# Performance work log

Measured on AMD Instinct MI355X. Metric: run time of the kernel, lower is better.

The kernel has to match this reference:

```python
import jax, jax.numpy as jnp
import numpy as np

B, R, C, E, H = 2, 16, 512, 1024, 16
D = E // H  # head_dim = 64


def setup_inputs() -> dict:
    key = jax.random.key(0)
    ks = jax.random.split(key, 9)
    s = 1.0 / np.sqrt(E)
    return {
        "x": jax.random.normal(ks[0], (B, R, C, E), dtype=jnp.float32),
        "wq": jax.random.uniform(ks[1], (E, E), jnp.float32, -s, s),
        "bq": jax.random.uniform(ks[2], (E,), jnp.float32, -s, s),
        "wk": jax.random.uniform(ks[3], (E, E), jnp.float32, -s, s),
        "bk": jax.random.uniform(ks[4], (E,), jnp.float32, -s, s),
        "wv": jax.random.uniform(ks[5], (E, E), jnp.float32, -s, s),
        "bv": jax.random.uniform(ks[6], (E,), jnp.float32, -s, s),
        "wo": jax.random.uniform(ks[7], (E, E), jnp.float32, -s, s),
        "bo": jax.random.uniform(ks[8], (E,), jnp.float32, -s, s),
    }


def reference(x, wq, bq, wk, bk, wv, bv, wo, bo):
    b, r, c, e = x.shape
    # projections: [b,r,c,e] -> [b,r,h,c,d]
    def split_heads(t):
        return t.reshape(b, r, c, H, D).transpose(0, 1, 3, 2, 4)
    q = split_heads(x @ wq + bq)
    k = split_heads(x @ wk + bk)
    v = split_heads(x @ wv + bv)
    scale = 1.0 / jnp.sqrt(jnp.asarray(D, x.dtype))
    logits = jnp.einsum('brhqd,brhkd->brhqk', q, k) * scale
    probs = jax.nn.softmax(logits, axis=-1)
    ctx = jnp.einsum('brhqk,brhkd->brhqd', probs, v)
    ctx = ctx.transpose(0, 1, 3, 2, 4).reshape(b, r, c, e)
    return ctx @ wo + bo
```

## Files before the change

kernel.cpp:

```cpp
#include <hip/hip_runtime.h>
#include <hip/hip_bf16.h>
#include <hip/hip_fp16.h>
#include <math.h>

typedef _Float16 half8 __attribute__((ext_vector_type(8)));
typedef __attribute__((ext_vector_type(4))) float floatx4;

constexpr int Bc = 2, Rc = 16, Cc = 512, Ec = 1024, Hc = 16, Dc = 64;
#define QSCALE 0.180336880111120425f

__device__ inline void gl_lds16(const void* g, void* l) {
  __builtin_amdgcn_global_load_lds(
      (const __attribute__((address_space(1))) void*)g,
      (__attribute__((address_space(3))) void*)l, 16, 0, 0);
}
__device__ inline unsigned short f2h(float f) {
  __half h = __float2half_rn(f);
  return *(unsigned short*)&h;
}
__device__ inline unsigned int pack_h2(float lo, float hi) {
  __half2 p = __float22half2_rn(make_float2(lo, hi));
  return *(unsigned int*)&p;
}

__global__ __launch_bounds__(256) void cvt_x(const float* __restrict__ x,
                                             unsigned short* __restrict__ xh) {
  const size_t base = ((size_t)blockIdx.x * 256 + threadIdx.x) * 8;
  float4 a = *(const float4*)(x + base);
  float4 b = *(const float4*)(x + base + 4);
  uint4 o;
  o.x = pack_h2(a.x, a.y);
  o.y = pack_h2(a.z, a.w);
  o.z = pack_h2(b.x, b.y);
  o.w = pack_h2(b.z, b.w);
  *(uint4*)(xh + base) = o;
}

__global__ __launch_bounds__(256) void wprep(
    const float* __restrict__ w0, const float* __restrict__ w1,
    const float* __restrict__ w2, const float* __restrict__ w3,
    unsigned short* __restrict__ t0, unsigned short* __restrict__ t1,
    unsigned short* __restrict__ t2, unsigned short* __restrict__ t3) {
  __shared__ float tile[64][65];
  const int z = blockIdx.z;
  const float* W = (z == 0) ? w0 : (z == 1) ? w1 : (z == 2) ? w2 : w3;
  unsigned short* T = (z == 0) ? t0 : (z == 1) ? t1 : (z == 2) ? t2 : t3;
  const int tid = threadIdx.x;
  const int bk = blockIdx.x * 64, bn = blockIdx.y * 64;
#pragma unroll
  for (int p = 0; p < 16; ++p) {
    int idx = p * 256 + tid;
    int lk = idx >> 6, lnn = idx & 63;
    tile[lnn][lk] = W[(size_t)(bk + lk) * 1024 + bn + lnn];
  }
  __syncthreads();
  const int lane = tid & 63, sub = tid >> 6;
  const int lr = lane & 15, quad = lane >> 4;
#pragma unroll
  for (int tl = 0; tl < 2; ++tl) {
    float v[8];
#pragma unroll
    for (int jj = 0; jj < 8; ++jj)
      v[jj] = tile[sub * 16 + lr][tl * 32 + quad * 8 + jj];
    uint4 o;
    o.x = pack_h2(v[0], v[1]);
    o.y = pack_h2(v[2], v[3]);
    o.z = pack_h2(v[4], v[5]);
    o.w = pack_h2(v[6], v[7]);
    const size_t n16 = (size_t)(bn >> 4) + sub;
    const size_t tt = (size_t)(bk >> 5) + tl;
    *(uint4*)(T + ((n16 * 32 + tt) * 64 + lane) * 8) = o;
  }
}

#define WAIT_VM(N)                                                            \
  {                                                                           \
    __builtin_amdgcn_sched_barrier(0);                                        \
    asm volatile("s_waitcnt vmcnt(" #N ")" ::: "memory");                     \
    __builtin_amdgcn_sched_barrier(0);                                        \
  }

#define STG_A(SBUF, KT)                                                       \
  {                                                                           \
    _Pragma("unroll") for (int l_ = 0; l_ < 2; ++l_) {                        \
      const int r0_ = l_ * 128 + w * 16;                                      \
      gl_lds16(Ab + (size_t)r0_ * 1024 + glan + (size_t)(KT) * 32,            \
               As + (SBUF) * 8192 + r0_ * 32);                                \
    }                                                                         \
  }

#define BLOAD(FB, KT)                                                         \
  _Pragma("unroll") for (int j_ = 0; j_ < 4; ++j_) FB[j_] =                   \
      *(const half8*)(Bf + bqoff + (size_t)j_ * 16384 + (size_t)(KT) * 512);

#define DSRA(NBUF, FA)                                                        \
  _Pragma("unroll") for (int i_ = 0; i_ < 8; ++i_) FA[i_] =                   \
      *(const half8*)&As[(NBUF) * 8192 + (wm + i_ * 16 + lr) * 32 + swq];

#define MFMA32(FA, FB)                                                        \
  _Pragma("unroll") for (int i_ = 0; i_ < 8; ++i_)                            \
      _Pragma("unroll") for (int j_ = 0; j_ < 4; ++j_) acc[i_][j_] =          \
          __builtin_amdgcn_mfma_f32_16x16x32_f16(FA[i_], FB[j_],              \
                                                 acc[i_][j_], 0, 0, 0);

#define TSTEP(NBUF, SBUF, KSTG, KBLD, FA, FB, NFA, NFB, STGE, BLDE, DSRE,     \
              VMN, BARE)                                                      \
  {                                                                           \
    if (STGE) STG_A(SBUF, KSTG);                                              \
    if (BLDE) BLOAD(NFB, KBLD);                                               \
    if (DSRE) DSRA(NBUF, NFA);                                                \
    WAIT_VM(VMN);                                                             \
    __builtin_amdgcn_s_setprio(1);                                            \
    MFMA32(FA, FB);                                                           \
    __builtin_amdgcn_s_setprio(0);                                            \
    if (BARE) {                                                               \
      __builtin_amdgcn_s_barrier();                                           \
      __builtin_amdgcn_sched_barrier(0);                                      \
    }                                                                         \
  }

template <int MODE>
__global__ __launch_bounds__(512, 2) void gemm256(
    const unsigned short* __restrict__ gA, const unsigned short* __restrict__ gB,
    const float* __restrict__ bq, const float* __restrict__ bk,
    const float* __restrict__ bv, unsigned short* __restrict__ qout,
    unsigned short* __restrict__ kout, unsigned short* __restrict__ vout,
    float* __restrict__ fout, const float* __restrict__ bo) {
  __shared__ unsigned short As[4 * 8192];
  const int tid = threadIdx.x;
  const int w = tid >> 6, ln = tid & 63;
  const int lr = ln & 15, quad = ln >> 4;
  const int wm = (w >> 2) * 128, wn = (w & 3) * 64;
  int bm, bn;
  if (MODE == 0) {
    const int swz = (blockIdx.x & 7) * 96 + (blockIdx.x >> 3);
    bm = (swz / 12) * 256;
    bn = (swz % 12) * 256;
  } else {
    const int swz = (blockIdx.x & 7) * 32 + (blockIdx.x >> 3);
    bm = (swz >> 2) * 256;
    bn = (swz & 3) * 256;
  }
  const unsigned short* Ab = gA + (size_t)bm * 1024;
  const unsigned short* Bf = gB;
  const size_t bqoff =
      (size_t)((bn >> 4) + (w & 3) * 4) * 16384 + (size_t)ln * 8;
  const int glan = (ln >> 2) * 1024 + (((ln & 3) ^ ((ln >> 3) & 3)) << 3);
  const int swq = ((quad ^ ((lr >> 1) & 3)) << 3);

  floatx4 acc[8][4];
#pragma unroll
  for (int i = 0; i < 8; ++i)
#pragma unroll
    for (int j = 0; j < 4; ++j) acc[i][j] = (floatx4)(0.f);
  half8 fa0[8], fa1[8], fb0[4], fb1[4];

  STG_A(0, 0);
  STG_A(1, 1);
  STG_A(2, 2);
  BLOAD(fb0, 0);
  WAIT_VM(6);
  __builtin_amdgcn_s_barrier();
  __builtin_amdgcn_sched_barrier(0);
  DSRA(0, fa0);

  for (int tt = 0; tt < 7; ++tt) {
    const int k4 = tt * 4;
    TSTEP(1, 3, k4 + 3, k4 + 1, fa0, fb0, fa1, fb1, 1, 1, 1, 6, 1);
    TSTEP(2, 0, k4 + 4, k4 + 2, fa1, fb1, fa0, fb0, 1, 1, 1, 6, 1);
    TSTEP(3, 1, k4 + 5, k4 + 3, fa0, fb0, fa1, fb1, 1, 1, 1, 6, 1);
    TSTEP(0, 2, k4 + 6, k4 + 4, fa1, fb1, fa0, fb0, 1, 1, 1, 6, 1);
  }
  TSTEP(1, 3, 31, 29, fa0, fb0, fa1, fb1, 1, 1, 1, 6, 1);
  TSTEP(2, 0, 0, 30, fa1, fb1, fa0, fb0, 0, 1, 1, 4, 1);
  TSTEP(3, 0, 0, 31, fa0, fb0, fa1, fb1, 0, 1, 1, 4, 1);
  TSTEP(0, 0, 0, 0, fa1, fb1, fa0, fb0, 0, 0, 0, 0, 0);

  const int q4 = quad * 4;
  const bool odd = ln & 1;
  if constexpr (MODE == 0) {
    const int z = bn >> 10;
    const float* bias = (z == 0) ? bq : (z == 1) ? bk : bv;
    const int czb = (bn & 1023) + wn;
#pragma unroll
    for (int i = 0; i < 8; ++i) {
#pragma unroll
      for (int j = 0; j < 4; ++j) {
        const int colz = czb + j * 16 + lr;
        float v[4];
#pragma unroll
        for (int r = 0; r < 4; ++r) v[r] = acc[i][j][r] + bias[colz];
        const int m0 = bm + wm + i * 16 + q4;
        const int h = colz >> 6, d = colz & 63;
        const int brr = m0 >> 9, c0 = m0 & 511;
        const size_t hb = ((size_t)brr * 16 + h) * 32768;
        if (z == 2) {
          uint2 o;
          o.x = pack_h2(v[0], v[1]);
          o.y = pack_h2(v[2], v[3]);
          *(uint2*)(vout + hb + (size_t)d * 512 + c0) = o;
        } else {
          unsigned short* outp = (z == 0) ? qout : kout;
          if (z == 0) {
#pragma unroll
            for (int r = 0; r < 4; ++r) v[r] *= QSCALE;
          }
#pragma unroll
          for (int rp = 0; rp < 2; ++rp) {
            float a = v[2 * rp], b = v[2 * rp + 1];
            float ax = __shfl_xor(a, 1), bx = __shfl_xor(b, 1);
            unsigned int u = odd ? pack_h2(bx, b) : pack_h2(a, ax);
            const int c = c0 + 2 * rp + (odd ? 1 : 0);
            const int dd = d & ~1;
            *(unsigned int*)(outp + hb + (size_t)c * 64 + dd) = u;
          }
        }
      }
    }
  } else {
#pragma unroll
    for (int i = 0; i < 8; ++i)
#pragma unroll
      for (int j = 0; j < 4; ++j) {
        const int col = bn + wn + j * 16 + lr;
#pragma unroll
        for (int r = 0; r < 4; ++r) {
          const int m = bm + wm + i * 16 + q4 + r;
          fout[(size_t)m * 1024 + col] = acc[i][j][r] + bo[col];
        }
      }
  }
}

__global__ __launch_bounds__(256, 2) void attn_mfma(
    const unsigned short* __restrict__ Qh, const unsigned short* __restrict__ Kb,
    const unsigned short* __restrict__ Vt, unsigned short* __restrict__ Ctx) {
  __shared__ unsigned short Ks[128 * 64];
  __shared__ unsigned short Vs[64 * 128];
  __shared__ unsigned short Ps[128][136];

  const int t = threadIdx.x;
  const int w = t >> 6, ln = t & 63;
  const int lane15 = ln & 15, quad = ln >> 4;
  const bool odd = ln & 1;
  const int bh = blockIdx.x >> 2;
  const int qb = (blockIdx.x & 3) * 128;

  half8 qf[2][2];
  {
    const size_t qbase =
        ((size_t)bh * 512 + qb + w * 32 + lane15) * 64 + quad * 8;
#pragma unroll
    for (int i = 0; i < 2; ++i)
#pragma unroll
      for (int c = 0; c < 2; ++c)
        qf[i][c] = *(const half8*)(Qh + qbase + (size_t)i * 16 * 64 + c * 32);
  }

  floatx4 oacc[2][4];
#pragma unroll
  for (int i = 0; i < 2; ++i)
#pragma unroll
    for (int dj = 0; dj < 4; ++dj) oacc[i][dj] = (floatx4)(0.f);
  float lsum[2][4];
#pragma unroll
  for (int i = 0; i < 2; ++i)
#pragma unroll
    for (int r = 0; r < 4; ++r) lsum[i][r] = 0.f;

  const unsigned short* kgb = Kb + (size_t)bh * 32768;
  const unsigned short* vgb = Vt + (size_t)bh * 32768;

  for (int kt = 0; kt < 512; kt += 128) {
    __syncthreads();
    {
      const unsigned short* kq = kgb + (size_t)kt * 64;
#pragma unroll
      for (int p = 0; p < 4; ++p) {
        const int s = p * 256 + t;
        const int kr = s >> 3, kc16 = s & 7;
        gl_lds16(kq + kr * 64 + ((kc16 ^ (kr & 7)) << 3), (char*)Ks + s * 16);
        const int vr = s >> 4, vc16 = s & 15;
        gl_lds16(vgb + vr * 512 + kt + ((vc16 ^ (vr & 15)) << 3),
                 (char*)Vs + s * 16);
      }
    }
    __syncthreads();

    floatx4 sacc[2][8];
#pragma unroll
    for (int i = 0; i < 2; ++i)
#pragma unroll
      for (int j = 0; j < 8; ++j) sacc[i][j] = (floatx4)(0.f);
#pragma unroll
    for (int j = 0; j < 8; ++j) {
      const int krow = j * 16 + lane15;
      const unsigned short* kr = Ks + krow * 64;
      half8 kf0 = *(const half8*)(kr + ((quad ^ (krow & 7)) << 3));
      half8 kf1 = *(const half8*)(kr + (((4 + quad) ^ (krow & 7)) << 3));
#pragma unroll
      for (int i = 0; i < 2; ++i) {
        sacc[i][j] = __builtin_amdgcn_mfma_f32_16x16x32_f16(qf[i][0], kf0,
                                                            sacc[i][j], 0, 0, 0);
        sacc[i][j] = __builtin_amdgcn_mfma_f32_16x16x32_f16(qf[i][1], kf1,
                                                            sacc[i][j], 0, 0, 0);
      }
    }

#pragma unroll
    for (int i = 0; i < 2; ++i) {
#pragma unroll
      for (int rp = 0; rp < 2; ++rp) {
        const int rA = rp * 2, rB = rA + 1;
        const int row = w * 32 + i * 16 + quad * 4 + rA + (odd ? 1 : 0);
        unsigned short* prow = &Ps[row][lane15 & ~1];
#pragma unroll
        for (int j = 0; j < 8; ++j) {
          const float pA = exp2f(sacc[i][j][rA]);
          const float pB = exp2f(sacc[i][j][rB]);
          lsum[i][rA] += pA;
          lsum[i][rB] += pB;
          const float an = __shfl_xor(pA, 1);
          const float bn = __shfl_xor(pB, 1);
          const float lo = odd ? bn : pA;
          const float hi = odd ? pB : an;
          *(unsigned int*)(prow + j * 16) = pack_h2(lo, hi);
        }
      }
    }

#pragma unroll
    for (int kc = 0; kc < 4; ++kc) {
      half8 pa0 = *(const half8*)&Ps[w * 32 + lane15][kc * 32 + quad * 8];
      half8 pa1 = *(const half8*)&Ps[w * 32 + 16 + lane15][kc * 32 + quad * 8];
#pragma unroll
      for (int dj = 0; dj < 4; ++dj) {
        const int drow = dj * 16 + lane15;
        half8 vf = *(const half8*)(
            Vs + drow * 128 + (((kc * 4 + quad) ^ (drow & 15)) << 3));
        oacc[0][dj] = __builtin_amdgcn_mfma_f32_16x16x32_f16(pa0, vf,
                                                             oacc[0][dj], 0, 0, 0);
        oacc[1][dj] = __builtin_amdgcn_mfma_f32_16x16x32_f16(pa1, vf,
                                                             oacc[1][dj], 0, 0, 0);
      }
    }
  }

  float invl[2][4];
#pragma unroll
  for (int i = 0; i < 2; ++i)
#pragma unroll
    for (int r = 0; r < 4; ++r) {
      float ls = lsum[i][r];
#pragma unroll
      for (int off = 1; off < 16; off <<= 1) ls += __shfl_xor(ls, off);
      invl[i][r] = 1.f / ls;
    }
  const int br = bh >> 4, h = bh & 15;
  const size_t mbase = (size_t)br * 512 + qb + w * 32;
#pragma unroll
  for (int i = 0; i < 2; ++i)
#pragma unroll
    for (int dj = 0; dj < 4; ++dj) {
      const int e = h * 64 + dj * 16 + lane15;
      const int ee = e & ~1;
#pragma unroll
      for (int rp = 0; rp < 2; ++rp) {
        const int rA = 2 * rp, rB = rA + 1;
        float a = oacc[i][dj][rA] * invl[i][rA];
        float b = oacc[i][dj][rB] * invl[i][rB];
        float ax = __shfl_xor(a, 1), bx = __shfl_xor(b, 1);
        unsigned int u = odd ? pack_h2(bx, b) : pack_h2(a, ax);
        const size_t m = mbase + i * 16 + quad * 4 + rA + (odd ? 1 : 0);
        *(unsigned int*)(Ctx + m * 1024 + ee) = u;
      }
    }
}

extern "C" void kernel_launch(void* const* d_in, const int* in_sizes, int n_in,
                              void* d_out, int out_size, void* d_ws,
                              size_t ws_size, hipStream_t stream) {
  const float* x = (const float*)d_in[0];
  const float* wq = (const float*)d_in[1];
  const float* bq = (const float*)d_in[2];
  const float* wk = (const float*)d_in[3];
  const float* bk = (const float*)d_in[4];
  const float* wv = (const float*)d_in[5];
  const float* bv = (const float*)d_in[6];
  const float* wo = (const float*)d_in[7];
  const float* bo = (const float*)d_in[8];
  float* out = (float*)d_out;

  char* w = (char*)d_ws;
  const size_t MiB = 1ull << 20;
  unsigned short* qbuf = (unsigned short*)(w + 0 * MiB);
  unsigned short* kbuf = (unsigned short*)(w + 32 * MiB);
  unsigned short* vtb = (unsigned short*)(w + 64 * MiB);
  unsigned short* xh = (unsigned short*)(w + 96 * MiB);
  unsigned short* ctx = (unsigned short*)(w + 128 * MiB);
  unsigned short* wqh = (unsigned short*)(w + 160 * MiB);
  unsigned short* wkh = (unsigned short*)(w + 162 * MiB);
  unsigned short* wvh = (unsigned short*)(w + 164 * MiB);
  unsigned short* woh = (unsigned short*)(w + 166 * MiB);

  cvt_x<<<8192, 256, 0, stream>>>(x, xh);
  wprep<<<dim3(16, 16, 4), 256, 0, stream>>>(wq, wk, wv, wo, wqh, wkh, wvh,
                                             woh);

  gemm256<0><<<768, 512, 0, stream>>>(xh, wqh, bq, bk, bv, qbuf, kbuf, vtb,
                                      nullptr, nullptr);

  attn_mfma<<<2048, 256, 0, stream>>>(qbuf, kbuf, vtb, ctx);

  gemm256<1><<<256, 512, 0, stream>>>(ctx, woh, nullptr, nullptr, nullptr,
                                      nullptr, nullptr, nullptr, out, bo);
}
```

Baseline: 371.8 us.

## Stage B operand through LDS with async loads and regroup block swizzle

Loads the B (weight) fragments into a new LDS ring buffer with global_load_lds instead of direct global-to-register loads, so both operands share one 4-slot async pipeline with a deeper prefetch distance. Waits on lgkmcnt are added before barriers, and the prologue stages four slots. The block-to-tile mapping is also changed so each XCD handles a contiguous group of M rows across a small set of N tiles, aiming for better L2 reuse. LDS use doubles, which may reduce occupancy, and the extra LDS round-trip for B adds ds_read traffic.

Result: slower. 431.5 us (+16.1%).

```diff
diff --git a/kernel.cpp b/kernel.cpp
--- a/kernel.cpp
+++ b/kernel.cpp
@@ -79,23 +79,34 @@
     asm volatile("s_waitcnt vmcnt(" #N ")" ::: "memory");                     \
     __builtin_amdgcn_sched_barrier(0);                                        \
   }
-
-#define STG_A(SBUF, KT)                                                       \
+#define WAIT_LGKM0                                                            \
+  {                                                                           \
+    asm volatile("s_waitcnt lgkmcnt(0)" ::: "memory");                        \
+    __builtin_amdgcn_sched_barrier(0);                                        \
+  }
+
+#define STG_AB(SLOT, KT)                                                      \
   {                                                                           \
     _Pragma("unroll") for (int l_ = 0; l_ < 2; ++l_) {                        \
       const int r0_ = l_ * 128 + w * 16;                                      \
       gl_lds16(Ab + (size_t)r0_ * 1024 + glan + (size_t)(KT) * 32,            \
-               As + (SBUF) * 8192 + r0_ * 32);                                \
+               As + (SLOT) * 8192 + r0_ * 32);                                \
     }                                                                         \
-  }
-
-#define BLOAD(FB, KT)                                                         \
-  _Pragma("unroll") for (int j_ = 0; j_ < 4; ++j_) FB[j_] =                   \
-      *(const half8*)(Bf + bqoff + (size_t)j_ * 16384 + (size_t)(KT) * 512);
-
-#define DSRA(NBUF, FA)                                                        \
-  _Pragma("unroll") for (int i_ = 0; i_ < 8; ++i_) FA[i_] =                   \
-      *(const half8*)&As[(NBUF) * 8192 + (wm + i_ * 16 + lr) * 32 + swq];
+    _Pragma("unroll") for (int l_ = 0; l_ < 2; ++l_) {                        \
+      const int fr_ = 2 * w + l_;                                             \
+      gl_lds16(Bf + (size_t)((n16b + fr_) * 32 + (KT)) * 512 + ln * 8,        \
+               Bs + (SLOT) * 8192 + fr_ * 512);                               \
+    }                                                                         \
+  }
+
+#define DSR(SLOT, FA, FB)                                                     \
+  {                                                                           \
+    _Pragma("unroll") for (int i_ = 0; i_ < 8; ++i_) FA[i_] =                 \
+        *(const half8*)&As[(SLOT) * 8192 + (wm + i_ * 16 + lr) * 32 + swq];   \
+    _Pragma("unroll") for (int j_ = 0; j_ < 4; ++j_) FB[j_] =                 \
+        *(const half8*)&Bs[(SLOT) * 8192 + ((w & 3) * 4 + j_) * 512 +         \
+                           ln * 8];                                           \
+  }
 
 #define MFMA32(FA, FB)                                                        \
   _Pragma("unroll") for (int i_ = 0; i_ < 8; ++i_)                            \
@@ -103,17 +114,18 @@
           __builtin_amdgcn_mfma_f32_16x16x32_f16(FA[i_], FB[j_],              \
                                                  acc[i_][j_], 0, 0, 0);
 
-#define TSTEP(NBUF, SBUF, KSTG, KBLD, FA, FB, NFA, NFB, STGE, BLDE, DSRE,     \
-              VMN, BARE)                                                      \
+#define TSTEP(DSLOT, SSLOT, KSTG, FA, FB, NFA, NFB, STGE, DSRE, VMW, BARE)    \
   {                                                                           \
-    if (STGE) STG_A(SBUF, KSTG);                                              \
-    if (BLDE) BLOAD(NFB, KBLD);                                               \
-    if (DSRE) DSRA(NBUF, NFA);                                                \
-    WAIT_VM(VMN);                                                             \
+    if (STGE) { STG_AB(SSLOT, KSTG); }                                        \
+    if (DSRE) { DSR(DSLOT, NFA, NFB); }                                       \
+    if ((VMW) == 0) { WAIT_VM(8); }                                           \
+    else if ((VMW) == 1) { WAIT_VM(4); }                                      \
+    else if ((VMW) == 2) { WAIT_VM(0); }                                      \
     __builtin_amdgcn_s_setprio(1);                                            \
     MFMA32(FA, FB);                                                           \
     __builtin_amdgcn_s_setprio(0);                                            \
     if (BARE) {                                                               \
+      WAIT_LGKM0;                                                             \
       __builtin_amdgcn_s_barrier();                                           \
       __builtin_amdgcn_sched_barrier(0);                                      \
     }                                                                         \
@@ -127,24 +139,25 @@
     unsigned short* __restrict__ kout, unsigned short* __restrict__ vout,
     float* __restrict__ fout, const float* __restrict__ bo) {
   __shared__ unsigned short As[4 * 8192];
+  __shared__ unsigned short Bs[4 * 8192];
   const int tid = threadIdx.x;
   const int w = tid >> 6, ln = tid & 63;
   const int lr = ln & 15, quad = ln >> 4;
   const int wm = (w >> 2) * 128, wn = (w & 3) * 64;
   int bm, bn;
   if (MODE == 0) {
-    const int swz = (blockIdx.x & 7) * 96 + (blockIdx.x >> 3);
-    bm = (swz / 12) * 256;
-    bn = (swz % 12) * 256;
+    const int xcd = blockIdx.x & 7, idx = blockIdx.x >> 3;
+    const int bng = idx >> 5, wi = idx & 31;
+    bm = (xcd * 8 + (wi >> 2)) * 256;
+    bn = (bng * 4 + (wi & 3)) * 256;
   } else {
-    const int swz = (blockIdx.x & 7) * 32 + (blockIdx.x >> 3);
-    bm = (swz >> 2) * 256;
-    bn = (swz & 3) * 256;
+    const int xcd = blockIdx.x & 7, idx = blockIdx.x >> 3;
+    bm = (xcd * 8 + (idx >> 2)) * 256;
+    bn = (idx & 3) * 256;
   }
   const unsigned short* Ab = gA + (size_t)bm * 1024;
   const unsigned short* Bf = gB;
-  const size_t bqoff =
-      (size_t)((bn >> 4) + (w & 3) * 4) * 16384 + (size_t)ln * 8;
+  const int n16b = bn >> 4;
   const int glan = (ln >> 2) * 1024 + (((ln & 3) ^ ((ln >> 3) & 3)) << 3);
   const int swq = ((quad ^ ((lr >> 1) & 3)) << 3);
 
@@ -155,26 +168,29 @@
     for (int j = 0; j < 4; ++j) acc[i][j] = (floatx4)(0.f);
   half8 fa0[8], fa1[8], fb0[4], fb1[4];
 
-  STG_A(0, 0);
-  STG_A(1, 1);
-  STG_A(2, 2);
-  BLOAD(fb0, 0);
-  WAIT_VM(6);
+  STG_AB(0, 0);
+  STG_AB(1, 1);
+  STG_AB(2, 2);
+  STG_AB(3, 3);
+  WAIT_VM(8);
   __builtin_amdgcn_s_barrier();
   __builtin_amdgcn_sched_barrier(0);
-  DSRA(0, fa0);
+  DSR(0, fa0, fb0);
+  WAIT_LGKM0;
+  __builtin_amdgcn_s_barrier();
+  __builtin_amdgcn_sched_barrier(0);
 
   for (int tt = 0; tt < 7; ++tt) {
     const int k4 = tt * 4;
-    TSTEP(1, 3, k4 + 3, k4 + 1, fa0, fb0, fa1, fb1, 1, 1, 1, 6, 1);
-    TSTEP(2, 0, k4 + 4, k4 + 2, fa1, fb1, fa0, fb0, 1, 1, 1, 6, 1);
-    TSTEP(3, 1, k4 + 5, k4 + 3, fa0, fb0, fa1, fb1, 1, 1, 1, 6, 1);
-    TSTEP(0, 2, k4 + 6, k4 + 4, fa1, fb1, fa0, fb0, 1, 1, 1, 6, 1);
-  }
-  TSTEP(1, 3, 31, 29, fa0, fb0, fa1, fb1, 1, 1, 1, 6, 1);
-  TSTEP(2, 0, 0, 30, fa1, fb1, fa0, fb0, 0, 1, 1, 4, 1);
-  TSTEP(3, 0, 0, 31, fa0, fb0, fa1, fb1, 0, 1, 1, 4, 1);
-  TSTEP(0, 0, 0, 0, fa1, fb1, fa0, fb0, 0, 0, 0, 0, 0);
+    TSTEP(1, 0, k4 + 4, fa0, fb0, fa1, fb1, 1, 1, 0, 1);
+    TSTEP(2, 1, k4 + 5, fa1, fb1, fa0, fb0, 1, 1, 0, 1);
+    TSTEP(3, 2, k4 + 6, fa0, fb0, fa1, fb1, 1, 1, 0, 1);
+    TSTEP(0, 3, k4 + 7, fa1, fb1, fa0, fb0, 1, 1, 0, 1);
+  }
+  TSTEP(1, 0, 0, fa0, fb0, fa1, fb1, 0, 1, 1, 1);
+  TSTEP(2, 0, 0, fa1, fb1, fa0, fb0, 0, 1, 2, 1);
+  TSTEP(3, 0, 0, fa0, fb0, fa1, fb1, 0, 1, 3, 1);
+  TSTEP(0, 0, 0, fa1, fb1, fa0, fb0, 0, 0, 3, 0);
 
   const int q4 = quad * 4;
   const bool odd = ln & 1;
```

## Prefetch next K/V tile into registers to overlap loads with attention compute

Applied to the files above, without the earlier changes.

Replaces the direct global-to-LDS async loads with a register-staged software pipeline. The next K/V tile is loaded into registers before computing the current tile, then written to swizzled LDS after a barrier at the end of the iteration. This hides global memory latency behind the MFMA work but adds register pressure and per-thread LDS stores in place of the direct-to-LDS path.

New measurement: 406.5 us. 9.3% more time.

```diff
diff --git a/kernel.cpp b/kernel.cpp
--- a/kernel.cpp
+++ b/kernel.cpp
@@ -271,21 +271,37 @@
   const unsigned short* kgb = Kb + (size_t)bh * 32768;
   const unsigned short* vgb = Vt + (size_t)bh * 32768;
 
+  uint4 kreg[4], vreg[4];
+#define AT_LOAD(KT)                                                           \
+  {                                                                           \
+    _Pragma("unroll") for (int p_ = 0; p_ < 4; ++p_) {                        \
+      const int s_ = p_ * 256 + t;                                            \
+      kreg[p_] = *(const uint4*)((const char*)kgb + (size_t)(KT) * 128 +      \
+                                 (size_t)s_ * 16);                            \
+      vreg[p_] = *(const uint4*)((const char*)vgb + (size_t)(KT) * 2 +        \
+                                 (size_t)(s_ >> 4) * 1024 + (s_ & 15) * 16);  \
+    }                                                                         \
+  }
+#define AT_WRITE                                                              \
+  {                                                                           \
+    _Pragma("unroll") for (int p_ = 0; p_ < 4; ++p_) {                        \
+      const int s_ = p_ * 256 + t;                                            \
+      const int kr_ = s_ >> 3, kc_ = s_ & 7;                                  \
+      *(uint4*)((char*)Ks + kr_ * 128 + ((kc_ ^ (kr_ & 7)) << 4)) = kreg[p_]; \
+      const int vr_ = s_ >> 4, vc_ = s_ & 15;                                 \
+      *(uint4*)((char*)Vs + vr_ * 256 + ((vc_ ^ (vr_ & 15)) << 4)) = vreg[p_];\
+    }                                                                         \
+  }
+
+  AT_LOAD(0);
+  AT_WRITE;
+
   for (int kt = 0; kt < 512; kt += 128) {
     __syncthreads();
-    {
-      const unsigned short* kq = kgb + (size_t)kt * 64;
-#pragma unroll
-      for (int p = 0; p < 4; ++p) {
-        const int s = p * 256 + t;
-        const int kr = s >> 3, kc16 = s & 7;
-        gl_lds16(kq + kr * 64 + ((kc16 ^ (kr & 7)) << 3), (char*)Ks + s * 16);
-        const int vr = s >> 4, vc16 = s & 15;
-        gl_lds16(vgb + vr * 512 + kt + ((vc16 ^ (vr & 15)) << 3),
-                 (char*)Vs + s * 16);
-      }
-    }
-    __syncthreads();
+    if (kt < 384) {
+      AT_LOAD(kt + 128);
+      __builtin_amdgcn_sched_barrier(0);
+    }
 
     floatx4 sacc[2][8];
 #pragma unroll
@@ -344,6 +360,9 @@
                                                              oacc[1][dj], 0, 0, 0);
       }
     }
+
+    __syncthreads();
+    if (kt < 384) AT_WRITE;
   }
 
   float invl[2][4];
```

## Prefetch next K/V tile into registers during PV MFMA and remap blocks

Applied to the files above, without the earlier changes.

The attention kernel now loads the next K/V tile from global memory into registers while the current tile's PV matmul runs, then writes it to LDS after a barrier. This replaces the synchronous global_load_lds path and is meant to hide load latency. It also remaps blockIdx so consecutive blocks spread across heads and query tiles, and raises wave priority around the MFMA sections. The cost is higher register pressure, which may hurt occupancy at launch_bounds(256,2).

Measured after the change: 362.6 us. -2.5%, faster.

```diff
diff --git a/kernel.cpp b/kernel.cpp
--- a/kernel.cpp
+++ b/kernel.cpp
@@ -243,8 +243,8 @@
   const int w = t >> 6, ln = t & 63;
   const int lane15 = ln & 15, quad = ln >> 4;
   const bool odd = ln & 1;
-  const int bh = blockIdx.x >> 2;
-  const int qb = (blockIdx.x & 3) * 128;
+  const int bh = (blockIdx.x & 7) * 64 + (blockIdx.x >> 5);
+  const int qb = ((blockIdx.x >> 3) & 3) * 128;
 
   half8 qf[2][2];
   {
@@ -271,27 +271,48 @@
   const unsigned short* kgb = Kb + (size_t)bh * 32768;
   const unsigned short* vgb = Vt + (size_t)bh * 32768;
 
-  for (int kt = 0; kt < 512; kt += 128) {
+  uint4 k0r, k1r, k2r, k3r, v0r, v1r, v2r, v3r;
+#define LDK(P, KT)                                                            \
+  (*(const uint4*)((const char*)kgb + (size_t)(KT) * 128 +                    \
+                   (size_t)((P) * 256 + t) * 16))
+#define LDV(P, KT)                                                            \
+  (*(const uint4*)((const char*)vgb + (size_t)(KT) * 2 +                      \
+                   (size_t)(((P) * 256 + t) >> 4) * 1024 +                    \
+                   (((P) * 256 + t) & 15) * 16))
+#define AT_LOAD(KT)                                                           \
+  {                                                                           \
+    k0r = LDK(0, KT); k1r = LDK(1, KT); k2r = LDK(2, KT); k3r = LDK(3, KT);   \
+    v0r = LDV(0, KT); v1r = LDV(1, KT); v2r = LDV(2, KT); v3r = LDV(3, KT);   \
+  }
+#define STK(P, R)                                                             \
+  {                                                                           \
+    const int s_ = (P) * 256 + t, kr_ = s_ >> 3, kc_ = s_ & 7;                \
+    *(uint4*)((char*)Ks + kr_ * 128 + ((kc_ ^ (kr_ & 7)) << 4)) = R;          \
+  }
+#define STV(P, R)                                                             \
+  {                                                                           \
+    const int s_ = (P) * 256 + t, vr_ = s_ >> 4, vc_ = s_ & 15;               \
+    *(uint4*)((char*)Vs + vr_ * 256 + ((vc_ ^ (vr_ & 15)) << 4)) = R;         \
+  }
+#define AT_WRITE                                                              \
+  {                                                                           \
+    STK(0, k0r); STK(1, k1r); STK(2, k2r); STK(3, k3r);                       \
+    STV(0, v0r); STV(1, v1r); STV(2, v2r); STV(3, v3r);                       \
+  }
+
+  AT_LOAD(0);
+  AT_WRITE;
+
+#pragma unroll
+  for (int ktt = 0; ktt < 4; ++ktt) {
     __syncthreads();
-    {
-      const unsigned short* kq = kgb + (size_t)kt * 64;
-#pragma unroll
-      for (int p = 0; p < 4; ++p) {
-        const int s = p * 256 + t;
-        const int kr = s >> 3, kc16 = s & 7;
-        gl_lds16(kq + kr * 64 + ((kc16 ^ (kr & 7)) << 3), (char*)Ks + s * 16);
-        const int vr = s >> 4, vc16 = s & 15;
-        gl_lds16(vgb + vr * 512 + kt + ((vc16 ^ (vr & 15)) << 3),
-                 (char*)Vs + s * 16);
-      }
-    }
-    __syncthreads();
 
     floatx4 sacc[2][8];
 #pragma unroll
     for (int i = 0; i < 2; ++i)
 #pragma unroll
       for (int j = 0; j < 8; ++j) sacc[i][j] = (floatx4)(0.f);
+    __builtin_amdgcn_s_setprio(1);
 #pragma unroll
     for (int j = 0; j < 8; ++j) {
       const int krow = j * 16 + lane15;
@@ -306,6 +327,7 @@
                                                             sacc[i][j], 0, 0, 0);
       }
     }
+    __builtin_amdgcn_s_setprio(0);
 
 #pragma unroll
     for (int i = 0; i < 2; ++i) {
@@ -329,6 +351,12 @@
       }
     }
 
+    if (ktt < 3) {
+      AT_LOAD((ktt + 1) * 128);
+      __builtin_amdgcn_sched_barrier(0);
+    }
+
+    __builtin_amdgcn_s_setprio(1);
 #pragma unroll
     for (int kc = 0; kc < 4; ++kc) {
       half8 pa0 = *(const half8*)&Ps[w * 32 + lane15][kc * 32 + quad * 8];
@@ -344,6 +372,10 @@
                                                              oacc[1][dj], 0, 0, 0);
       }
     }
+    __builtin_amdgcn_s_setprio(0);
+
+    __syncthreads();
+    if (ktt < 3) AT_WRITE;
   }
 
   float invl[2][4];
```
